# Kernel optimization log

Measured on AMD Instinct MI355X. Metric: run time of the kernel, lower is better.

## Reference

```python
import jax, jax.numpy as jnp
import numpy as np

B, S, H = 1, 2048, 2048
NH = 16
Q_LORA, KV_LORA = 1536, 512
D_NOPE, D_ROPE, D_V = 128, 64, 128
D_QK = D_NOPE + D_ROPE  # 192
EPS = 1e-6
ROPE_BASE = 10000.0


def setup_inputs() -> dict:
    key = jax.random.key(0)
    ks = jax.random.split(key, 8)
    def lin(k, fan_in, fan_out):
        # nn.Linear default init, stored as [in, out] for x @ W
        bound = 1.0 / np.sqrt(fan_in)
        return jax.random.uniform(k, (fan_in, fan_out), jnp.float32, -bound, bound)
    return {
        "hidden_states": jax.random.normal(ks[0], (B, S, H), jnp.float32),
        "Wqa": lin(ks[1], H, Q_LORA),
        "q_a_ln_w": jnp.ones((Q_LORA,), jnp.float32),
        "Wqb": lin(ks[2], Q_LORA, NH * D_QK),
        "Wkva": lin(ks[3], H, KV_LORA + D_ROPE),
        "kv_a_ln_w": jnp.ones((KV_LORA,), jnp.float32),
        "Wkvb": lin(ks[4], KV_LORA, NH * (D_NOPE + D_V)),
        "Wo": lin(ks[5], NH * D_V, H),
    }


def _rmsnorm(x, w):
    xf = x.astype(jnp.float32)
    var = jnp.mean(xf * xf, axis=-1, keepdims=True)
    return w * (xf * jax.lax.rsqrt(var + EPS)).astype(x.dtype)


def _rotate_half(x):
    x1, x2 = jnp.split(x, 2, axis=-1)
    return jnp.concatenate((-x2, x1), axis=-1)


def _rope_tables(seq_len, dtype=jnp.float32):
    inv_freq = 1.0 / (ROPE_BASE ** (jnp.arange(0, D_ROPE, 2, dtype=jnp.float32) / D_ROPE))
    t = jnp.arange(seq_len, dtype=jnp.float32)
    freqs = jnp.outer(t, inv_freq)                      # [S, D_ROPE/2]
    emb = jnp.concatenate((freqs, freqs), axis=-1)      # [S, D_ROPE]
    return jnp.cos(emb).astype(dtype), jnp.sin(emb).astype(dtype)


def reference(hidden_states, Wqa, q_a_ln_w, Wqb, Wkva, kv_a_ln_w, Wkvb, Wo):
    bsz, q_len, _ = hidden_states.shape
    scale = D_QK ** -0.5

    # Q path: LoRA down -> RMSNorm -> up
    q = _rmsnorm(hidden_states @ Wqa, q_a_ln_w) @ Wqb            # [B,S,NH*D_QK]
    q = q.reshape(bsz, q_len, NH, D_QK).transpose(0, 2, 1, 3)    # [B,NH,S,D_QK]
    q_nope, q_pe = q[..., :D_NOPE], q[..., D_NOPE:]

    # KV path: compressed latent + shared rope key
    ckv = hidden_states @ Wkva                                    # [B,S,KV_LORA+D_ROPE]
    compressed_kv, k_pe = ckv[..., :KV_LORA], ckv[..., KV_LORA:]
    k_pe = k_pe.reshape(bsz, q_len, 1, D_ROPE).transpose(0, 2, 1, 3)  # [B,1,S,D_ROPE]
    kv = _rmsnorm(compressed_kv, kv_a_ln_w) @ Wkvb                # [B,S,NH*(D_NOPE+D_V)]
    kv = kv.reshape(bsz, q_len, NH, D_NOPE + D_V).transpose(0, 2, 1, 3)
    k_nope, v = kv[..., :D_NOPE], kv[..., D_NOPE:]                # [B,NH,S,D_NOPE], [B,NH,S,D_V]

    # decoupled RoPE on the rope sub-dims
    cos, sin = _rope_tables(q_len, hidden_states.dtype)
    cos = cos[None, None]  # [1,1,S,D_ROPE] broadcast over batch & heads
    sin = sin[None, None]
    q_pe = q_pe * cos + _rotate_half(q_pe) * sin
    k_pe = k_pe * cos + _rotate_half(k_pe) * sin                  # [B,1,S,D_ROPE]

    query = jnp.concatenate([q_nope, q_pe], axis=-1)              # [B,NH,S,D_QK]
    key = jnp.concatenate([k_nope, jnp.broadcast_to(k_pe, (bsz, NH, q_len, D_ROPE))], axis=-1)

    attn = jnp.einsum('bhqd,bhkd->bhqk', query, key) * scale      # [B,NH,S,S]
    causal = jnp.triu(jnp.ones((q_len, q_len), bool), k=1)
    attn = jnp.where(causal, -jnp.inf, attn)
    attn = jax.nn.softmax(attn.astype(jnp.float32), axis=-1).astype(query.dtype)

    out = jnp.einsum('bhqk,bhkd->bhqd', attn, v)                  # [B,NH,S,D_V]
    out = out.transpose(0, 2, 1, 3).reshape(bsz, q_len, NH * D_V)
    return out @ Wo                                               # [B,S,H]
```

## Files before the change

### kernel.cpp

```cpp
#include <hip/hip_runtime.h>
#include <hip/hip_bf16.h>
#include <math.h>

#define S_LEN 2048
#define H_DIM 2048
#define NH 16
#define Q_LORA 1536
#define KV_LORA 512
#define D_NOPE 128
#define D_ROPE 64
#define D_V 128
#define D_QK 192

typedef unsigned short ushort_t;
typedef __attribute__((ext_vector_type(8))) short short8;
typedef __attribute__((ext_vector_type(4))) float f32x4;

__device__ __forceinline__ ushort_t f2bf(float f) {
    unsigned int u = __float_as_uint(f);
    u = (u + 0x7FFFu + ((u >> 16) & 1u)) >> 16;
    return (ushort_t)u;
}
__device__ __forceinline__ float bf2f(ushort_t u) {
    return __uint_as_float(((unsigned int)u) << 16);
}

__device__ __forceinline__ void storeC(float* p, float v) { *p = v; }
__device__ __forceinline__ void storeC(ushort_t* p, float v) { *p = f2bf(v); }

__device__ __forceinline__ void gload_lds16(const ushort_t* g, ushort_t* l) {
    __builtin_amdgcn_global_load_lds(
        (const __attribute__((address_space(1))) unsigned int*)(const void*)g,
        (__attribute__((address_space(3))) unsigned int*)(void*)l, 16, 0, 0);
}

__device__ __forceinline__ float dpp_max16(float x) {
    x = fmaxf(x, __int_as_float(__builtin_amdgcn_update_dpp(0, __float_as_int(x), 0xB1, 0xF, 0xF, true)));
    x = fmaxf(x, __int_as_float(__builtin_amdgcn_update_dpp(0, __float_as_int(x), 0x4E, 0xF, 0xF, true)));
    x = fmaxf(x, __int_as_float(__builtin_amdgcn_update_dpp(0, __float_as_int(x), 0x124, 0xF, 0xF, true)));
    x = fmaxf(x, __int_as_float(__builtin_amdgcn_update_dpp(0, __float_as_int(x), 0x128, 0xF, 0xF, true)));
    return x;
}
__device__ __forceinline__ float dpp_sum16(float x) {
    x += __int_as_float(__builtin_amdgcn_update_dpp(0, __float_as_int(x), 0xB1, 0xF, 0xF, true));
    x += __int_as_float(__builtin_amdgcn_update_dpp(0, __float_as_int(x), 0x4E, 0xF, 0xF, true));
    x += __int_as_float(__builtin_amdgcn_update_dpp(0, __float_as_int(x), 0x124, 0xF, 0xF, true));
    x += __int_as_float(__builtin_amdgcn_update_dpp(0, __float_as_int(x), 0x128, 0xF, 0xF, true));
    return x;
}

__global__ __launch_bounds__(256) void conv_f32_bf16(
    const float* __restrict__ X, ushort_t* __restrict__ Y, int n)
{
    int base = (blockIdx.x * 256 + threadIdx.x) * 4;
    if (base >= n) return;
    float4 v = *(const float4*)(X + base);
    Y[base + 0] = f2bf(v.x);
    Y[base + 1] = f2bf(v.y);
    Y[base + 2] = f2bf(v.z);
    Y[base + 3] = f2bf(v.w);
}

__global__ __launch_bounds__(256) void convT_kernel(
    const float* __restrict__ W, ushort_t* __restrict__ Wt, int K, int N)
{
    __shared__ float tile[32][33];
    const int k0 = blockIdx.y * 32, n0 = blockIdx.x * 32;
    const int tr = threadIdx.x >> 5, tc = threadIdx.x & 31;
    #pragma unroll
    for (int i = 0; i < 4; ++i) {
        int r = tr + i * 8;
        float v = 0.f;
        if (n0 + tc < N) v = W[(size_t)(k0 + r) * N + n0 + tc];
        tile[r][tc] = v;
    }
    __syncthreads();
    #pragma unroll
    for (int i = 0; i < 4; ++i) {
        int r = tr + i * 8;
        Wt[(size_t)(n0 + r) * K + k0 + tc] = f2bf(tile[tc][r]);
    }
}

__global__ __launch_bounds__(256) void fused_norm_ropek(
    const ushort_t* __restrict__ cat16r, ushort_t* __restrict__ qa16,
    ushort_t* __restrict__ ckv16n, ushort_t* __restrict__ kpe16,
    const float* __restrict__ qlnw, const float* __restrict__ klnw)
{
    __shared__ float red[4];
    const int b = blockIdx.x;
    if (b < 4096) {
        const bool isQ = (b < 2048);
        const int row = isQ ? b : b - 2048;
        const int K = isQ ? Q_LORA : KV_LORA;
        const ushort_t* x = cat16r + (size_t)row * 2176 + (isQ ? 0 : Q_LORA);
        ushort_t* y = (isQ ? qa16 + (size_t)row * Q_LORA : ckv16n + (size_t)row * KV_LORA);
        const float* wv = isQ ? qlnw : klnw;
        float ss = 0.f;
        for (int i = threadIdx.x; i < K; i += 256) { float v = bf2f(x[i]); ss += v * v; }
        #pragma unroll
        for (int off = 32; off > 0; off >>= 1) ss += __shfl_down(ss, off);
        int lane = threadIdx.x & 63, wid = threadIdx.x >> 6;
        if (lane == 0) red[wid] = ss;
        __syncthreads();
        float tot = red[0] + red[1] + red[2] + red[3];
        float rs = rsqrtf(tot / (float)K + 1e-6f);
        for (int i = threadIdx.x; i < K; i += 256)
            y[i] = f2bf(bf2f(x[i]) * rs * wv[i]);
    } else {
        int idx = (b - 4096) * 256 + threadIdx.x;
        if (idx >= S_LEN * 32) return;
        int i = idx & 31;
        int s = idx >> 5;
        float inv = powf(10000.0f, -(2.0f * i) / 64.0f);
        float ang = (float)s * inv;
        float c = cosf(ang), sn = sinf(ang);
        const ushort_t* p = cat16r + (size_t)s * 2176 + Q_LORA + KV_LORA;
        ushort_t* q = kpe16 + (size_t)s * D_ROPE;
        float x1 = bf2f(p[i]), x2 = bf2f(p[i + 32]);
        q[i]      = f2bf(x1 * c - x2 * sn);
        q[i + 32] = f2bf(x2 * c + x1 * sn);
    }
}

__global__ void rope_bf16_kernel(
    ushort_t* __restrict__ X, int rowStride, int dimOffset, int headStride, int nHeads)
{
    int idx = blockIdx.x * 256 + threadIdx.x;
    if (idx >= S_LEN * nHeads * 32) return;
    int i = idx & 31;
    int sh = idx >> 5;
    int hh = sh % nHeads;
    int s = sh / nHeads;
    float inv = powf(10000.0f, -(2.0f * i) / 64.0f);
    float ang = (float)s * inv;
    float c = cosf(ang), sn = sinf(ang);
    ushort_t* p = X + (size_t)s * rowStride + hh * headStride + dimOffset;
    float x1 = bf2f(p[i]), x2 = bf2f(p[i + 32]);
    p[i]      = f2bf(x1 * c - x2 * sn);
    p[i + 32] = f2bf(x2 * c + x1 * sn);
}

__global__ __launch_bounds__(256) void conv_vT_kernel(
    const ushort_t* __restrict__ kv, ushort_t* __restrict__ v16t)
{
    __shared__ ushort_t tile[32][33];
    const int h = blockIdx.z;
    const int s0 = blockIdx.x * 32, d0 = blockIdx.y * 32;
    const int tr = threadIdx.x >> 5, tc = threadIdx.x & 31;
    #pragma unroll
    for (int i = 0; i < 4; ++i) {
        int r = tr + i * 8;
        tile[r][tc] = kv[(size_t)(s0 + r) * 4096 + h * 256 + D_NOPE + d0 + tc];
    }
    __syncthreads();
    #pragma unroll
    for (int i = 0; i < 4; ++i) {
        int r = tr + i * 8;
        v16t[(size_t)h * D_V * S_LEN + (size_t)(d0 + r) * S_LEN + s0 + tc] = tile[tc][r];
    }
}

template <typename CT>
__device__ __forceinline__ void gemm_body_bk64(
    const ushort_t* __restrict__ A, const ushort_t* __restrict__ Bt,
    CT* __restrict__ C, int N, int K, int m0, int n0,
    ushort_t* Al, ushort_t* Bl)
{
    const int tid = threadIdx.x;
    const int lane = tid & 63;
    const int w = tid >> 6;
    const int lm = lane & 15, quad = lane >> 4;
    const int wr = w >> 1, wc = w & 1;

    f32x4 acc[2][4];
    #pragma unroll
    for (int a = 0; a < 2; ++a)
        #pragma unroll
        for (int b = 0; b < 4; ++b) acc[a][b] = (f32x4){0.f, 0.f, 0.f, 0.f};

    const int rrow = tid >> 2;
    const int rcol = (tid & 3) * 8;

    for (int k0 = 0; k0 < K; k0 += 64) {
        __syncthreads();
        #pragma unroll
        for (int c = 0; c < 2; ++c) {
            gload_lds16(A + (size_t)(m0 + rrow) * K + k0 + c * 32 + rcol,
                        Al + c * 2048 + tid * 8);
            #pragma unroll
            for (int i = 0; i < 2; ++i)
                gload_lds16(Bt + (size_t)(n0 + i * 64 + rrow) * K + k0 + c * 32 + rcol,
                            Bl + c * 4096 + (i * 256 + tid) * 8);
        }
        __syncthreads();

        #pragma unroll
        for (int c = 0; c < 2; ++c) {
            short8 af[2], bf[4];
            #pragma unroll
            for (int t = 0; t < 2; ++t)
                af[t] = *(const short8*)(Al + c * 2048 + (wr * 32 + t * 16 + lm) * 32 + quad * 8);
            #pragma unroll
            for (int t = 0; t < 4; ++t)
                bf[t] = *(const short8*)(Bl + c * 4096 + (wc * 64 + t * 16 + lm) * 32 + quad * 8);
            #pragma unroll
            for (int mt = 0; mt < 2; ++mt)
                #pragma unroll
                for (int nt = 0; nt < 4; ++nt)
                    acc[mt][nt] = __builtin_amdgcn_mfma_f32_16x16x32_bf16(
                        af[mt], bf[nt], acc[mt][nt], 0, 0, 0);
        }
    }

    #pragma unroll
    for (int mt = 0; mt < 2; ++mt)
        #pragma unroll
        for (int nt = 0; nt < 4; ++nt)
            #pragma unroll
            for (int r = 0; r < 4; ++r) {
                int row = m0 + wr * 32 + mt * 16 + quad * 4 + r;
                int col = n0 + wc * 64 + nt * 16 + lm;
                storeC(&C[(size_t)row * N + col], acc[mt][nt][r]);
            }
}

template <typename CT>
__global__ __launch_bounds__(256) void mfma_gemm_bt(
    const ushort_t* __restrict__ A, const ushort_t* __restrict__ Bt,
    CT* __restrict__ C, int N, int K)
{
    __shared__ ushort_t Al[2 * 64 * 32];
    __shared__ ushort_t Bl[2 * 128 * 32];
    gemm_body_bk64<CT>(A, Bt, C, N, K, blockIdx.y * 64, blockIdx.x * 128, Al, Bl);
}

__global__ __launch_bounds__(256) void mfma_gemm_dual(
    const ushort_t* __restrict__ A1, const ushort_t* __restrict__ Bt1,
    ushort_t* __restrict__ C1, int N1, int K1, int nb1,
    const ushort_t* __restrict__ A2, const ushort_t* __restrict__ Bt2,
    ushort_t* __restrict__ C2, int N2, int K2)
{
    __shared__ ushort_t Al[2 * 64 * 32];
    __shared__ ushort_t Bl[2 * 128 * 32];
    int g = blockIdx.x;
    if (g < nb1) {
        int nbx = N1 / 128;
        gemm_body_bk64<ushort_t>(A1, Bt1, C1, N1, K1, (g / nbx) * 64, (g % nbx) * 128, Al, Bl);
    } else {
        g -= nb1;
        int nbx = N2 / 128;
        gemm_body_bk64<ushort_t>(A2, Bt2, C2, N2, K2, (g / nbx) * 64, (g % nbx) * 128, Al, Bl);
    }
}

__device__ __forceinline__ void softmax_step(
    f32x4 s[4], int k0, int qw, int lm, int quad,
    float m_[4], float l_[4], f32x4 O[8], ushort_t* ps)
{
    const float scale = 0.07216878364870322f;
    #pragma unroll
    for (int r = 0; r < 4; ++r) {
        int qrow = qw + quad * 4 + r;
        float a[4];
        #pragma unroll
        for (int st = 0; st < 4; ++st)
            a[st] = (k0 + st * 16 + lm <= qrow) ? s[st][r] * scale : -1e30f;
        float mx = dpp_max16(fmaxf(fmaxf(a[0], a[1]), fmaxf(a[2], a[3])));
        float mn = fmaxf(m_[r], mx);
        float p[4];
        #pragma unroll
        for (int st = 0; st < 4; ++st) p[st] = __expf(a[st] - mn);
        float alpha = __expf(m_[r] - mn);
        float psum = dpp_sum16((p[0] + p[1]) + (p[2] + p[3]));
        l_[r] = l_[r] * alpha + psum;
        m_[r] = mn;
        #pragma unroll
        for (int c = 0; c < 8; ++c) O[c][r] *= alpha;
        #pragma unroll
        for (int st = 0; st < 4; ++st)
            ps[(quad * 4 + r) * 72 + st * 16 + lm] = f2bf(p[st]);
    }
}

__global__ __launch_bounds__(128) void mla_attn_kernel(
    const ushort_t* __restrict__ qb, const ushort_t* __restrict__ kvb,
    const ushort_t* __restrict__ kpe, const ushort_t* __restrict__ v16t,
    ushort_t* __restrict__ aout16)
{
    __shared__ ushort_t Kn[4 * 64 * 32];
    __shared__ ushort_t Kr[2 * 64 * 32];
    __shared__ ushort_t Vt[2 * 128 * 32];
    __shared__ ushort_t Ps[2][16][72];

    const int h = blockIdx.x;
    const int q0 = 32 * (63 - blockIdx.y);
    const int w = threadIdx.x >> 6;
    const int lane = threadIdx.x & 63;
    const int lm = lane & 15, quad = lane >> 4;
    const int qw = q0 + 16 * w;
    ushort_t* myPs = &Ps[w][0][0];

    short8 qf[6];
    #pragma unroll
    for (int f = 0; f < 6; ++f)
        qf[f] = *(const short8*)(qb + (size_t)(qw + lm) * 3072 + h * 192 + f * 32 + quad * 8);

    f32x4 O[8];
    #pragma unroll
    for (int c = 0; c < 8; ++c) O[c] = (f32x4){0.f, 0.f, 0.f, 0.f};
    float m_[4] = {-1e30f, -1e30f, -1e30f, -1e30f};
    float l_[4] = {0.f, 0.f, 0.f, 0.f};

    const int skey = lane >> 2;
    const int ssub = (lane & 3) * 8;

    const int kend = q0 + 32;
    for (int k0 = 0; k0 < kend; k0 += 64) {
        __syncthreads();
        {
            #pragma unroll
            for (int fi = 0; fi < 2; ++fi) {
                int f = 2 * w + fi;
                #pragma unroll
                for (int i = 0; i < 4; ++i)
                    gload_lds16(kvb + (size_t)(k0 + i * 16 + skey) * 4096 + h * 256 + f * 32 + ssub,
                                Kn + f * 2048 + i * 512 + lane * 8);
            }
            #pragma unroll
            for (int i = 0; i < 4; ++i)
                gload_lds16(kpe + (size_t)(k0 + i * 16 + skey) * 64 + w * 32 + ssub,
                            Kr + w * 2048 + i * 512 + lane * 8);
            #pragma unroll
            for (int j = 0; j < 8; ++j)
                gload_lds16(v16t + ((size_t)h * 128 + j * 16 + skey) * S_LEN + k0 + w * 32 + ssub,
                            Vt + w * 4096 + j * 512 + lane * 8);
        }
        __syncthreads();

        if (k0 < qw + 16) {
            f32x4 s[4];
            #pragma unroll
            for (int st = 0; st < 4; ++st) s[st] = (f32x4){0.f, 0.f, 0.f, 0.f};
            #pragma unroll
            for (int f = 0; f < 4; ++f)
                #pragma unroll
                for (int st = 0; st < 4; ++st) {
                    short8 kf = *(const short8*)(Kn + f * 2048 + (st * 16 + lm) * 32 + quad * 8);
                    s[st] = __builtin_amdgcn_mfma_f32_16x16x32_bf16(qf[f], kf, s[st], 0, 0, 0);
                }
            #pragma unroll
            for (int f2 = 0; f2 < 2; ++f2)
                #pragma unroll
                for (int st = 0; st < 4; ++st) {
                    short8 kf = *(const short8*)(Kr + f2 * 2048 + (st * 16 + lm) * 32 + quad * 8);
                    s[st] = __builtin_amdgcn_mfma_f32_16x16x32_bf16(qf[4 + f2], kf, s[st], 0, 0, 0);
                }

            softmax_step(s, k0, qw, lm, quad, m_, l_, O, myPs);

            asm volatile("s_waitcnt lgkmcnt(0)" ::: "memory");
            short8 pf0 = *(const short8*)(myPs + lm * 72 + quad * 8);
            short8 pf1 = *(const short8*)(myPs + lm * 72 + 32 + quad * 8);
            #pragma unroll
            for (int c = 0; c < 8; ++c) {
                short8 vf0 = *(const short8*)(Vt + (c * 16 + lm) * 32 + quad * 8);
                short8 vf1 = *(const short8*)(Vt + 4096 + (c * 16 + lm) * 32 + quad * 8);
                O[c] = __builtin_amdgcn_mfma_f32_16x16x32_bf16(pf0, vf0, O[c], 0, 0, 0);
                O[c] = __builtin_amdgcn_mfma_f32_16x16x32_bf16(pf1, vf1, O[c], 0, 0, 0);
            }
        }
    }
    #pragma unroll
    for (int c = 0; c < 8; ++c)
        #pragma unroll
        for (int r = 0; r < 4; ++r) {
            int qrow = qw + quad * 4 + r;
            aout16[(size_t)qrow * 2048 + h * D_V + c * 16 + lm] = f2bf(O[c][r] / l_[r]);
        }
}

extern "C" void kernel_launch(void* const* d_in, const int* in_sizes, int n_in,
                              void* d_out, int out_size, void* d_ws, size_t ws_size,
                              hipStream_t stream)
{
    (void)in_sizes; (void)n_in; (void)out_size; (void)ws_size;
    const float* hs   = (const float*)d_in[0];
    const float* Wqa  = (const float*)d_in[1];
    const float* qlnw = (const float*)d_in[2];
    const float* Wqb  = (const float*)d_in[3];
    const float* Wkva = (const float*)d_in[4];
    const float* klnw = (const float*)d_in[5];
    const float* Wkvb = (const float*)d_in[6];
    const float* Wo   = (const float*)d_in[7];
    float* out = (float*)d_out;

    ushort_t* p = (ushort_t*)d_ws;
    ushort_t* hs16   = p; p += (size_t)S_LEN * H_DIM;
    ushort_t* WcatT  = p; p += (size_t)2176 * H_DIM;
    ushort_t* WqbT   = p; p += (size_t)3072 * Q_LORA;
    ushort_t* WkvbT  = p; p += (size_t)4096 * KV_LORA;
    ushort_t* WoT    = p; p += (size_t)H_DIM * H_DIM;
    ushort_t* cat16r = p; p += (size_t)S_LEN * 2176;
    ushort_t* qa16   = p; p += (size_t)S_LEN * Q_LORA;
    ushort_t* qbuf16 = p; p += (size_t)S_LEN * 3072;
    ushort_t* ckv16n = p; p += (size_t)S_LEN * KV_LORA;
    ushort_t* kpe16  = p; p += (size_t)S_LEN * D_ROPE;
    ushort_t* kv16   = p; p += (size_t)S_LEN * 4096;
    ushort_t* v16t   = p; p += (size_t)NH * D_V * S_LEN;
    ushort_t* aout16 = p; p += (size_t)S_LEN * 2048;

    conv_f32_bf16<<<(S_LEN * H_DIM / 4 + 255) / 256, 256, 0, stream>>>(hs, hs16, S_LEN * H_DIM);
    convT_kernel<<<dim3(Q_LORA / 32, H_DIM / 32), 256, 0, stream>>>(Wqa, WcatT, H_DIM, Q_LORA);
    convT_kernel<<<dim3(640 / 32, H_DIM / 32), 256, 0, stream>>>(
        Wkva, WcatT + (size_t)Q_LORA * H_DIM, H_DIM, 576);
    convT_kernel<<<dim3(3072 / 32, Q_LORA / 32), 256, 0, stream>>>(Wqb, WqbT, Q_LORA, 3072);
    convT_kernel<<<dim3(4096 / 32, KV_LORA / 32), 256, 0, stream>>>(Wkvb, WkvbT, KV_LORA, 4096);
    convT_kernel<<<dim3(H_DIM / 32, H_DIM / 32), 256, 0, stream>>>(Wo, WoT, H_DIM, H_DIM);

    mfma_gemm_bt<ushort_t><<<dim3(2176 / 128, S_LEN / 64), 256, 0, stream>>>(
        hs16, WcatT, cat16r, 2176, H_DIM);
    fused_norm_ropek<<<4096 + 256, 256, 0, stream>>>(cat16r, qa16, ckv16n, kpe16, qlnw, klnw);
    mfma_gemm_dual<<<768 + 1024, 256, 0, stream>>>(
        qa16, WqbT, qbuf16, 3072, Q_LORA, 768,
        ckv16n, WkvbT, kv16, 4096, KV_LORA);
    rope_bf16_kernel<<<(S_LEN * NH * 32 + 255) / 256, 256, 0, stream>>>(
        qbuf16, 3072, D_NOPE, D_QK, NH);
    conv_vT_kernel<<<dim3(S_LEN / 32, D_V / 32, NH), 256, 0, stream>>>(kv16, v16t);
    mla_attn_kernel<<<dim3(NH, 64), 128, 0, stream>>>(qbuf16, kv16, kpe16, v16t, aout16);
    mfma_gemm_bt<float><<<dim3(H_DIM / 128, S_LEN / 64), 256, 0, stream>>>(
        aout16, WoT, out, H_DIM, H_DIM);
}
```

Baseline: 353.2 us.

## Merge conversion launches, fuse query RoPE into attention, load rope keys directly

Replaces the six separate conversion/transpose launches with one unified kernel that dispatches on block index. Removes the standalone query RoPE kernel and applies the rotation to the q_pe fragments in registers at the start of the attention kernel. The shared rope-key slice is now read straight from global memory into registers instead of staged through LDS. This saves launches and a read-modify-write pass over the query buffer, at the cost of uncoalesced per-lane global loads of k_pe inside the attention loop and transcendental calls per attention thread.

```diff
diff --git a/kernel.cpp b/kernel.cpp
--- a/kernel.cpp
+++ b/kernel.cpp
@@ -49,23 +49,10 @@
     return x;
 }
 
-__global__ __launch_bounds__(256) void conv_f32_bf16(
-    const float* __restrict__ X, ushort_t* __restrict__ Y, int n)
-{
-    int base = (blockIdx.x * 256 + threadIdx.x) * 4;
-    if (base >= n) return;
-    float4 v = *(const float4*)(X + base);
-    Y[base + 0] = f2bf(v.x);
-    Y[base + 1] = f2bf(v.y);
-    Y[base + 2] = f2bf(v.z);
-    Y[base + 3] = f2bf(v.w);
-}
-
-__global__ __launch_bounds__(256) void convT_kernel(
-    const float* __restrict__ W, ushort_t* __restrict__ Wt, int K, int N)
-{
-    __shared__ float tile[32][33];
-    const int k0 = blockIdx.y * 32, n0 = blockIdx.x * 32;
+__device__ __forceinline__ void convT_body(
+    const float* __restrict__ W, ushort_t* __restrict__ Wt,
+    int K, int N, int n0, int k0, float (*tile)[33])
+{
     const int tr = threadIdx.x >> 5, tc = threadIdx.x & 31;
     #pragma unroll
     for (int i = 0; i < 4; ++i) {
@@ -80,6 +67,35 @@
         int r = tr + i * 8;
         Wt[(size_t)(n0 + r) * K + k0 + tc] = f2bf(tile[tc][r]);
     }
+}
+
+__global__ __launch_bounds__(256) void unified_conv(
+    const float* __restrict__ hs, ushort_t* __restrict__ hs16,
+    const float* __restrict__ Wqa, const float* __restrict__ Wkva,
+    const float* __restrict__ Wqb, const float* __restrict__ Wkvb,
+    const float* __restrict__ Wo,
+    ushort_t* __restrict__ WcatT, ushort_t* __restrict__ WqbT,
+    ushort_t* __restrict__ WkvbT, ushort_t* __restrict__ WoT)
+{
+    __shared__ float tile[32][33];
+    int b = blockIdx.x;
+    if (b < 4096) {
+        int base = (b * 256 + threadIdx.x) * 4;
+        float4 v = *(const float4*)(hs + base);
+        hs16[base + 0] = f2bf(v.x);
+        hs16[base + 1] = f2bf(v.y);
+        hs16[base + 2] = f2bf(v.z);
+        hs16[base + 3] = f2bf(v.w);
+        return;
+    }
+    b -= 4096;
+    const float* W; ushort_t* Wt; int K, N, nbx;
+    if (b < 3072)        {            W = Wqa;  Wt = WcatT;                              K = 2048; N = 1536; nbx = 48;  }
+    else if (b < 4352)   { b -= 3072; W = Wkva; Wt = WcatT + (size_t)Q_LORA * H_DIM;     K = 2048; N = 576;  nbx = 20;  }
+    else if (b < 8960)   { b -= 4352; W = Wqb;  Wt = WqbT;                               K = 1536; N = 3072; nbx = 96;  }
+    else if (b < 11008)  { b -= 8960; W = Wkvb; Wt = WkvbT;                              K = 512;  N = 4096; nbx = 128; }
+    else                 { b -= 11008; W = Wo;  Wt = WoT;                                K = 2048; N = 2048; nbx = 64;  }
+    convT_body(W, Wt, K, N, (b % nbx) * 32, (b / nbx) * 32, tile);
 }
 
 __global__ __launch_bounds__(256) void fused_norm_ropek(
@@ -123,24 +139,6 @@
     }
 }
 
-__global__ void rope_bf16_kernel(
-    ushort_t* __restrict__ X, int rowStride, int dimOffset, int headStride, int nHeads)
-{
-    int idx = blockIdx.x * 256 + threadIdx.x;
-    if (idx >= S_LEN * nHeads * 32) return;
-    int i = idx & 31;
-    int sh = idx >> 5;
-    int hh = sh % nHeads;
-    int s = sh / nHeads;
-    float inv = powf(10000.0f, -(2.0f * i) / 64.0f);
-    float ang = (float)s * inv;
-    float c = cosf(ang), sn = sinf(ang);
-    ushort_t* p = X + (size_t)s * rowStride + hh * headStride + dimOffset;
-    float x1 = bf2f(p[i]), x2 = bf2f(p[i + 32]);
-    p[i]      = f2bf(x1 * c - x2 * sn);
-    p[i + 32] = f2bf(x2 * c + x1 * sn);
-}
-
 __global__ __launch_bounds__(256) void conv_vT_kernel(
     const ushort_t* __restrict__ kv, ushort_t* __restrict__ v16t)
 {
@@ -289,7 +287,6 @@
     ushort_t* __restrict__ aout16)
 {
     __shared__ ushort_t Kn[4 * 64 * 32];
-    __shared__ ushort_t Kr[2 * 64 * 32];
     __shared__ ushort_t Vt[2 * 128 * 32];
     __shared__ ushort_t Ps[2][16][72];
 
@@ -305,6 +302,20 @@
     #pragma unroll
     for (int f = 0; f < 6; ++f)
         qf[f] = *(const short8*)(qb + (size_t)(qw + lm) * 3072 + h * 192 + f * 32 + quad * 8);
+    {
+        float srow = (float)(qw + lm);
+        #pragma unroll
+        for (int j = 0; j < 8; ++j) {
+            int i = quad * 8 + j;
+            float inv = powf(10000.0f, -(2.0f * i) / 64.0f);
+            float ang = srow * inv;
+            float c = cosf(ang), sn = sinf(ang);
+            float x1 = bf2f((ushort_t)qf[4][j]);
+            float x2 = bf2f((ushort_t)qf[5][j]);
+            qf[4][j] = (short)f2bf(x1 * c - x2 * sn);
+            qf[5][j] = (short)f2bf(x2 * c + x1 * sn);
+        }
+    }
 
     f32x4 O[8];
     #pragma unroll
@@ -318,6 +329,13 @@
     const int kend = q0 + 32;
     for (int k0 = 0; k0 < kend; k0 += 64) {
         __syncthreads();
+        short8 krf[2][4];
+        #pragma unroll
+        for (int st = 0; st < 4; ++st)
+            #pragma unroll
+            for (int f2 = 0; f2 < 2; ++f2)
+                krf[f2][st] = *(const short8*)(
+                    kpe + (size_t)(k0 + st * 16 + lm) * 64 + f2 * 32 + quad * 8);
         {
             #pragma unroll
             for (int fi = 0; fi < 2; ++fi) {
@@ -328,10 +346,6 @@
                                 Kn + f * 2048 + i * 512 + lane * 8);
             }
             #pragma unroll
-            for (int i = 0; i < 4; ++i)
-                gload_lds16(kpe + (size_t)(k0 + i * 16 + skey) * 64 + w * 32 + ssub,
-                            Kr + w * 2048 + i * 512 + lane * 8);
-            #pragma unroll
             for (int j = 0; j < 8; ++j)
                 gload_lds16(v16t + ((size_t)h * 128 + j * 16 + skey) * S_LEN + k0 + w * 32 + ssub,
                             Vt + w * 4096 + j * 512 + lane * 8);
@@ -352,10 +366,8 @@
             #pragma unroll
             for (int f2 = 0; f2 < 2; ++f2)
                 #pragma unroll
-                for (int st = 0; st < 4; ++st) {
-                    short8 kf = *(const short8*)(Kr + f2 * 2048 + (st * 16 + lm) * 32 + quad * 8);
-                    s[st] = __builtin_amdgcn_mfma_f32_16x16x32_bf16(qf[4 + f2], kf, s[st], 0, 0, 0);
-                }
+                for (int st = 0; st < 4; ++st)
+                    s[st] = __builtin_amdgcn_mfma_f32_16x16x32_bf16(qf[4 + f2], krf[f2][st], s[st], 0, 0, 0);
 
             softmax_step(s, k0, qw, lm, quad, m_, l_, O, myPs);
 
@@ -410,22 +422,14 @@
     ushort_t* v16t   = p; p += (size_t)NH * D_V * S_LEN;
     ushort_t* aout16 = p; p += (size_t)S_LEN * 2048;
 
-    conv_f32_bf16<<<(S_LEN * H_DIM / 4 + 255) / 256, 256, 0, stream>>>(hs, hs16, S_LEN * H_DIM);
-    convT_kernel<<<dim3(Q_LORA / 32, H_DIM / 32), 256, 0, stream>>>(Wqa, WcatT, H_DIM, Q_LORA);
-    convT_kernel<<<dim3(640 / 32, H_DIM / 32), 256, 0, stream>>>(
-        Wkva, WcatT + (size_t)Q_LORA * H_DIM, H_DIM, 576);
-    convT_kernel<<<dim3(3072 / 32, Q_LORA / 32), 256, 0, stream>>>(Wqb, WqbT, Q_LORA, 3072);
-    convT_kernel<<<dim3(4096 / 32, KV_LORA / 32), 256, 0, stream>>>(Wkvb, WkvbT, KV_LORA, 4096);
-    convT_kernel<<<dim3(H_DIM / 32, H_DIM / 32), 256, 0, stream>>>(Wo, WoT, H_DIM, H_DIM);
-
+    unified_conv<<<19200, 256, 0, stream>>>(
+        hs, hs16, Wqa, Wkva, Wqb, Wkvb, Wo, WcatT, WqbT, WkvbT, WoT);
     mfma_gemm_bt<ushort_t><<<dim3(2176 / 128, S_LEN / 64), 256, 0, stream>>>(
         hs16, WcatT, cat16r, 2176, H_DIM);
     fused_norm_ropek<<<4096 + 256, 256, 0, stream>>>(cat16r, qa16, ckv16n, kpe16, qlnw, klnw);
     mfma_gemm_dual<<<768 + 1024, 256, 0, stream>>>(
         qa16, WqbT, qbuf16, 3072, Q_LORA, 768,
         ckv16n, WkvbT, kv16, 4096, KV_LORA);
-    rope_bf16_kernel<<<(S_LEN * NH * 32 + 255) / 256, 256, 0, stream>>>(
-        qbuf16, 3072, D_NOPE, D_QK, NH);
     conv_vT_kernel<<<dim3(S_LEN / 32, D_V / 32, NH), 256, 0, stream>>>(kv16, v16t);
     mla_attn_kernel<<<dim3(NH, 64), 128, 0, stream>>>(qbuf16, kv16, kpe16, v16t, aout16);
     mfma_gemm_bt<float><<<dim3(H_DIM / 128, S_LEN / 64), 256, 0, stream>>>(
```

New measurement: 350.3 us. No clear change (-0.8%).
